# Kernel tuning notes

Measured on AMD Instinct MI355X. Metric: run time of the kernel, lower is better.

## Reference

```python
import jax, jax.numpy as jnp
import numpy as np

NUM_HEADS = 4
NUM_GROUPS = 32
EPS = 1e-5


def group_norm(x, gamma, beta):
    B, C, H, W = x.shape
    g = x.reshape(B, NUM_GROUPS, C // NUM_GROUPS, H, W)
    mean = g.mean(axis=(2, 3, 4), keepdims=True)
    var = g.var(axis=(2, 3, 4), keepdims=True)
    g = (g - mean) * jax.lax.rsqrt(var + EPS)
    x = g.reshape(B, C, H, W)
    return x * gamma[None, :, None, None] + beta[None, :, None, None]


def setup_inputs() -> dict:
    key = jax.random.key(0)
    ks = jax.random.split(key, 7)
    B, C, H, W = 16, 256, 32, 32
    x = jax.random.normal(ks[0], (B, C, H, W), dtype=jnp.float32)
    gn_gamma = jnp.ones((C,), dtype=jnp.float32)
    gn_beta = jnp.zeros((C,), dtype=jnp.float32)
    s = 1.0 / np.sqrt(C)
    qkv_w = jax.random.normal(ks[1], (3 * C, C), dtype=jnp.float32) * s
    qkv_b = jnp.zeros((3 * C,), dtype=jnp.float32)
    proj_w = jax.random.normal(ks[2], (C, C), dtype=jnp.float32) * s
    proj_b = jnp.zeros((C,), dtype=jnp.float32)
    return {"x": x, "gn_gamma": gn_gamma, "gn_beta": gn_beta,
            "qkv_w": qkv_w, "qkv_b": qkv_b, "proj_w": proj_w, "proj_b": proj_b}


def reference(x, gn_gamma, gn_beta, qkv_w, qkv_b, proj_w, proj_b):
    B, C, H, W = x.shape
    nh = NUM_HEADS
    d = C // nh
    N = H * W

    h = group_norm(x, gn_gamma, gn_beta)
    # 1x1 conv == channel matmul
    qkv = jnp.einsum('bchw,oc->bohw', h, qkv_w) + qkv_b[None, :, None, None]
    qkv = qkv.reshape(B, 3, nh, d, N)
    q, k, v = qkv[:, 0], qkv[:, 1], qkv[:, 2]  # each [B, nh, d, N]

    scale = 1.0 / jnp.sqrt(jnp.asarray(d, dtype=x.dtype))
    attn = jnp.einsum('bhdn,bhdm->bhnm', q, k) * scale  # [B, nh, N, N]
    attn = jax.nn.softmax(attn, axis=-1)
    out = jnp.einsum('bhnm,bhdm->bhdn', attn, v)  # [B, nh, d, N]
    out = out.reshape(B, C, H, W)

    out = jnp.einsum('bchw,oc->bohw', out, proj_w) + proj_b[None, :, None, None]
    return x + out
```

## Files before the change

kernel.cpp:

```cpp
#include <hip/hip_runtime.h>
#include <math.h>

typedef unsigned short u16;
typedef unsigned int u32;
typedef __attribute__((ext_vector_type(8))) short s16x8;
typedef __attribute__((ext_vector_type(4))) float f32x4;

#define NB 16
#define NN 1024
#define GN_EPS 1e-5f

static __device__ __forceinline__ u16 f2bf(float f) {
    union { float f; u32 u; } v; v.f = f;
    return (u16)((v.u + 0x8000u) >> 16);
}
static __device__ __forceinline__ u32 pk2(float a, float b) {
    union { float f; u32 u; } A, B; A.f = a; B.f = b;
    return __builtin_amdgcn_perm(A.u + 0x8000u, B.u + 0x8000u, 0x03020706u);
}

#define GLL16(gp, lp) __builtin_amdgcn_global_load_lds( \
    (const __attribute__((address_space(1))) void*)(const void*)(gp), \
    (__attribute__((address_space(3))) void*)(void*)(lp), 16, 0, 0)

__global__ __launch_bounds__(256) void gn_stats_kernel(
    const float* __restrict__ x, float2* __restrict__ stats)
{
    const int bg = blockIdx.x;
    const int t  = threadIdx.x;
    const float4* xb = (const float4*)(x + (size_t)bg * 8192);
    float s = 0.f, ss = 0.f;
#pragma unroll
    for (int i = 0; i < 8; ++i) {
        float4 f = xb[t + i * 256];
        s  += f.x + f.y + f.z + f.w;
        ss += f.x * f.x + f.y * f.y + f.z * f.z + f.w * f.w;
    }
#pragma unroll
    for (int off = 32; off > 0; off >>= 1) {
        s  += __shfl_down(s, off);
        ss += __shfl_down(ss, off);
    }
    __shared__ float red[8];
    const int wid = t >> 6;
    if ((t & 63) == 0) { red[wid] = s; red[4 + wid] = ss; }
    __syncthreads();
    if (t == 0) {
        float sa = red[0] + red[1] + red[2] + red[3];
        float sb = red[4] + red[5] + red[6] + red[7];
        float mean = sa * (1.0f / 8192.0f);
        float var  = sb * (1.0f / 8192.0f) - mean * mean;
        stats[bg] = make_float2(mean, 1.0f / sqrtf(var + GN_EPS));
    }
}

__global__ __launch_bounds__(256) void wcvt_kernel(
    const float* __restrict__ qkv_w, const float* __restrict__ proj_w,
    u16* __restrict__ wqb, u16* __restrict__ wpb)
{
    int i = blockIdx.x * 256 + threadIdx.x;
    if (i < 49152) {
        float4 f = ((const float4*)qkv_w)[i];
        *(uint2*)(wqb + (size_t)i * 4) = make_uint2(pk2(f.x, f.y), pk2(f.z, f.w));
    } else {
        int j = i - 49152;
        float4 f = ((const float4*)proj_w)[j];
        *(uint2*)(wpb + (size_t)j * 4) = make_uint2(pk2(f.x, f.y), pk2(f.z, f.w));
    }
}

__global__ __launch_bounds__(256) void gnorm_t_kernel(
    const float* __restrict__ x, const float2* __restrict__ stats,
    const float* __restrict__ gamma, const float* __restrict__ beta,
    u16* __restrict__ Xt)
{
    const int b = blockIdx.z, ct = blockIdx.y, nt = blockIdx.x;
    const int t = threadIdx.x;
    __shared__ float T[64][65];
    const float* xb = x + ((size_t)b * 256 + ct * 64) * NN + nt * 64;
#pragma unroll
    for (int i = 0; i < 4; ++i) {
        int row = i * 16 + (t >> 4), col = (t & 15) * 4;
        int ch = ct * 64 + row;
        float2 st = stats[b * 32 + (ch >> 3)];
        float gmv = st.y * gamma[ch];
        float btv = beta[ch] - st.x * gmv;
        float4 f = *(const float4*)&xb[(size_t)row * NN + col];
        T[row][col + 0] = f.x * gmv + btv;
        T[row][col + 1] = f.y * gmv + btv;
        T[row][col + 2] = f.z * gmv + btv;
        T[row][col + 3] = f.w * gmv + btv;
    }
    __syncthreads();
    u16* dst = Xt + ((size_t)b * NN + nt * 64) * 256 + ct * 64;
#pragma unroll
    for (int p = 0; p < 2; ++p) {
        int idx = t + p * 256;
        int nl = idx >> 3, c8 = idx & 7;
        s16x8 pv;
#pragma unroll
        for (int j = 0; j < 8; ++j) pv[j] = (short)f2bf(T[c8 * 8 + j][nl]);
        *(s16x8*)(dst + (size_t)nl * 256 + c8 * 8) = pv;
    }
}

__global__ __launch_bounds__(256) void qkv_mfma_kernel(
    const u16* __restrict__ Wb, const float* __restrict__ bias,
    const u16* __restrict__ Xt,
    u16* __restrict__ qh, u16* __restrict__ kh, u16* __restrict__ vh)
{
    const int b = blockIdx.z, ot = blockIdx.y, nt = blockIdx.x;
    const int t = threadIdx.x, w = t >> 6, l = t & 63;
    const int g = l >> 4, c = l & 15;
    __shared__ u16 Slds[32 * 512];
    const u16* Xb = Xt + ((size_t)b * NN + nt * 128) * 256;
    const u16* Wo = Wb + (size_t)ot * 64 * 256;
    const int part = ot >> 2, h = ot & 3;
    const size_t bhoff = (size_t)(b * 4 + h) << 16;

    if (part < 2) {
#pragma unroll
        for (int s = w; s < 32; s += 4) {
            int osub = s >> 3, ks = s & 7;
            GLL16(Wo + (size_t)(osub * 16 + c) * 256 + ks * 32 + g * 8, Slds + s * 512);
        }
        s16x8 a0[8], a1[8];
#pragma unroll
        for (int ks = 0; ks < 8; ++ks) {
            a0[ks] = *(const s16x8*)(Xb + (size_t)((2 * w) * 16 + c) * 256 + ks * 32 + g * 8);
            a1[ks] = *(const s16x8*)(Xb + (size_t)((2 * w + 1) * 16 + c) * 256 + ks * 32 + g * 8);
        }
        f32x4 acc[2][4];
#pragma unroll
        for (int i = 0; i < 2; ++i)
#pragma unroll
            for (int j = 0; j < 4; ++j) acc[i][j] = (f32x4){0.f, 0.f, 0.f, 0.f};
        __syncthreads();
#pragma unroll
        for (int ks = 0; ks < 8; ++ks)
#pragma unroll
            for (int j = 0; j < 4; ++j) {
                s16x8 bf = *(const s16x8*)(Slds + (j * 8 + ks) * 512 + l * 8);
                acc[0][j] = __builtin_amdgcn_mfma_f32_16x16x32_bf16(a0[ks], bf, acc[0][j], 0, 0, 0);
                acc[1][j] = __builtin_amdgcn_mfma_f32_16x16x32_bf16(a1[ks], bf, acc[1][j], 0, 0, 0);
            }
        const float sc = (part == 0) ? 0.125f * 1.44269504088896f : 1.0f;
        float bv[4];
#pragma unroll
        for (int j = 0; j < 4; ++j) bv[j] = bias[ot * 64 + j * 16 + c];
        u16* dst = (part == 0 ? qh : kh) + bhoff + (size_t)(nt * 128) * 64;
#pragma unroll
        for (int i = 0; i < 2; ++i)
#pragma unroll
            for (int j = 0; j < 4; ++j)
#pragma unroll
                for (int r = 0; r < 4; ++r) {
                    int n = (2 * w + i) * 16 + g * 4 + r;
                    dst[(size_t)n * 64 + j * 16 + c] = f2bf((acc[i][j][r] + bv[j]) * sc);
                }
    } else {
        f32x4 acc[8];
#pragma unroll
        for (int j = 0; j < 8; ++j) acc[j] = (f32x4){0.f, 0.f, 0.f, 0.f};
        for (int kk = 0; kk < 256; kk += 128) {
            if (kk) __syncthreads();
#pragma unroll
            for (int s = w; s < 32; s += 4) {
                int nsub = s >> 2, ks = s & 3;
                GLL16(Xb + (size_t)(nsub * 16 + c) * 256 + kk + ks * 32 + g * 8, Slds + s * 512);
            }
            __syncthreads();
#pragma unroll
            for (int ks = 0; ks < 4; ++ks) {
                s16x8 a = *(const s16x8*)(Wo + (size_t)(w * 16 + c) * 256 + kk + ks * 32 + g * 8);
#pragma unroll
                for (int j = 0; j < 8; ++j) {
                    s16x8 xf = *(const s16x8*)(Slds + (j * 4 + ks) * 512 + l * 8);
                    acc[j] = __builtin_amdgcn_mfma_f32_16x16x32_bf16(a, xf, acc[j], 0, 0, 0);
                }
            }
        }
        float bv[4];
#pragma unroll
        for (int r = 0; r < 4; ++r) bv[r] = bias[ot * 64 + w * 16 + g * 4 + r];
        u16* dst = vh + bhoff;
#pragma unroll
        for (int j = 0; j < 8; ++j)
#pragma unroll
            for (int r = 0; r < 4; ++r) {
                int d = w * 16 + g * 4 + r;
                int m = nt * 128 + j * 16 + c;
                dst[(size_t)d * NN + m] = f2bf(acc[j][r] + bv[r]);
            }
    }
}

__global__ __launch_bounds__(512) void attn_mfma_kernel(
    const u16* __restrict__ qh, const u16* __restrict__ kh,
    const u16* __restrict__ vh, u16* __restrict__ aoT)
{
    const int t = threadIdx.x;
    const int w = t >> 6, l = t & 63;
    const int g = l >> 4, c = l & 15;
    const int bid = blockIdx.x;
    const int xcd = bid & 7;
    const int idx = bid >> 3;
    const int qt  = idx & 7;
    const int grp = (idx >> 3) * 8 + xcd;
    const int b = grp >> 2, h = grp & 3;
    const size_t bhoff = (size_t)grp << 16;
    const int n_base = qt * 128 + w * 16;

    __shared__ u16 Klds[2][8 * 512];
    __shared__ u16 Vlds[2][8 * 512];
    __shared__ u16 Plds[8][2 * 512];

    const u16* qb = qh + bhoff;
    const u16* kb = kh + bhoff;
    const u16* vb = vh + bhoff;

    const int msub = w >> 1, uu = w & 1;

    s16x8 qf[2];
#pragma unroll
    for (int u = 0; u < 2; ++u)
        qf[u] = *(const s16x8*)(qb + (size_t)(n_base + c) * 64 + u * 32 + g * 8);

    s16x8 onef;
#pragma unroll
    for (int j = 0; j < 8; ++j) onef[j] = (short)0x3F80;

    f32x4 Oacc[4];
    f32x4 Lacc = (f32x4){0.f, 0.f, 0.f, 0.f};
#pragma unroll
    for (int ds = 0; ds < 4; ++ds) Oacc[ds] = (f32x4){0.f, 0.f, 0.f, 0.f};

    u16* pw = &Plds[w][0];

    GLL16(kb + (size_t)(msub * 16 + c) * 64 + uu * 32 + g * 8, &Klds[0][w * 512]);
    GLL16(vb + (size_t)(msub * 16 + c) * NN + uu * 32 + g * 8, &Vlds[0][w * 512]);

    for (int mt = 0; mt < 16; ++mt) {
        const int cur = mt & 1;
        if (mt < 15) {
            const int m1 = (mt + 1) * 64;
            GLL16(kb + (size_t)(m1 + msub * 16 + c) * 64 + uu * 32 + g * 8, &Klds[cur ^ 1][w * 512]);
            GLL16(vb + (size_t)(msub * 16 + c) * NN + m1 + uu * 32 + g * 8, &Vlds[cur ^ 1][w * 512]);
            asm volatile("s_waitcnt vmcnt(2)" ::: "memory");
        } else {
            asm volatile("s_waitcnt vmcnt(0)" ::: "memory");
        }
        __builtin_amdgcn_s_barrier();
        asm volatile("" ::: "memory");

        const u16* Kc = &Klds[cur][0];
        const u16* Vc = &Vlds[cur][0];

        f32x4 S[4];
#pragma unroll
        for (int ms = 0; ms < 4; ++ms) S[ms] = (f32x4){0.f, 0.f, 0.f, 0.f};
#pragma unroll
        for (int ms = 0; ms < 4; ++ms)
#pragma unroll
            for (int u = 0; u < 2; ++u) {
                s16x8 af = *(const s16x8*)(Kc + (ms * 2 + u) * 512 + l * 8);
                S[ms] = __builtin_amdgcn_mfma_f32_16x16x32_bf16(af, qf[u], S[ms], 0, 0, 0);
            }

        s16x8 vf[4][2];
#pragma unroll
        for (int ds = 0; ds < 4; ++ds)
#pragma unroll
            for (int u = 0; u < 2; ++u)
                vf[ds][u] = *(const s16x8*)(Vc + (ds * 2 + u) * 512 + l * 8);

#pragma unroll
        for (int ms = 0; ms < 4; ++ms)
#pragma unroll
            for (int r = 0; r < 4; ++r) S[ms][r] = __builtin_amdgcn_exp2f(S[ms][r]);

#pragma unroll
        for (int ms = 0; ms < 4; ++ms) {
            u32 d0 = pk2(S[ms][0], S[ms][1]);
            u32 d1 = pk2(S[ms][2], S[ms][3]);
            int off = (ms >> 1) * 512 + ((ms & 1) * 2 + (g >> 1)) * 128 + c * 8 + (g & 1) * 4;
            *(uint2*)(pw + off) = make_uint2(d0, d1);
        }
        asm volatile("s_waitcnt lgkmcnt(0)" ::: "memory");
#pragma unroll
        for (int u = 0; u < 2; ++u) {
            s16x8 pf = *(const s16x8*)(pw + u * 512 + l * 8);
#pragma unroll
            for (int ds = 0; ds < 4; ++ds)
                Oacc[ds] = __builtin_amdgcn_mfma_f32_16x16x32_bf16(vf[ds][u], pf, Oacc[ds], 0, 0, 0);
            Lacc = __builtin_amdgcn_mfma_f32_16x16x32_bf16(onef, pf, Lacc, 0, 0, 0);
        }
        asm volatile("" ::: "memory");
        __builtin_amdgcn_s_barrier();
    }

    u16* aob = aoT + (size_t)b * NN * 256 + h * 64;
    float inv = 1.0f / Lacc[0];
    const size_t nrow = (size_t)(n_base + c) * 256;
#pragma unroll
    for (int ds = 0; ds < 4; ++ds) {
        u32 lo = pk2(Oacc[ds][0] * inv, Oacc[ds][1] * inv);
        u32 hi = pk2(Oacc[ds][2] * inv, Oacc[ds][3] * inv);
        *(uint2*)(aob + nrow + ds * 16 + g * 4) = make_uint2(lo, hi);
    }
}

__global__ __launch_bounds__(256) void proj_mfma_kernel(
    const u16* __restrict__ Wb, const float* __restrict__ bias,
    const u16* __restrict__ aoT, const float* __restrict__ x,
    float* __restrict__ out)
{
    const int b = blockIdx.z, ot = blockIdx.y, nt = blockIdx.x;
    const int t = threadIdx.x, w = t >> 6, l = t & 63;
    const int g = l >> 4, c = l & 15;
    __shared__ u16 Slds[32 * 512];
    const u16* Xb = aoT + ((size_t)b * NN + nt * 128) * 256;
    const u16* Wo = Wb + (size_t)ot * 64 * 256;

    f32x4 acc[8];
#pragma unroll
    for (int j = 0; j < 8; ++j) acc[j] = (f32x4){0.f, 0.f, 0.f, 0.f};
    for (int kk = 0; kk < 256; kk += 128) {
        if (kk) __syncthreads();
#pragma unroll
        for (int s = w; s < 32; s += 4) {
            int nsub = s >> 2, ks = s & 3;
            GLL16(Xb + (size_t)(nsub * 16 + c) * 256 + kk + ks * 32 + g * 8, Slds + s * 512);
        }
        __syncthreads();
#pragma unroll
        for (int ks = 0; ks < 4; ++ks) {
            s16x8 a = *(const s16x8*)(Wo + (size_t)(w * 16 + c) * 256 + kk + ks * 32 + g * 8);
#pragma unroll
            for (int j = 0; j < 8; ++j) {
                s16x8 xf = *(const s16x8*)(Slds + (j * 4 + ks) * 512 + l * 8);
                acc[j] = __builtin_amdgcn_mfma_f32_16x16x32_bf16(a, xf, acc[j], 0, 0, 0);
            }
        }
    }
    float bv[4];
#pragma unroll
    for (int r = 0; r < 4; ++r) bv[r] = bias[ot * 64 + w * 16 + g * 4 + r];
#pragma unroll
    for (int j = 0; j < 8; ++j)
#pragma unroll
        for (int r = 0; r < 4; ++r) {
            int o = ot * 64 + w * 16 + g * 4 + r;
            int n = nt * 128 + j * 16 + c;
            size_t addr = ((size_t)b * 256 + o) * NN + n;
            out[addr] = acc[j][r] + bv[r] + x[addr];
        }
}

extern "C" void kernel_launch(void* const* d_in, const int* in_sizes, int n_in,
                              void* d_out, int out_size, void* d_ws, size_t ws_size,
                              hipStream_t stream)
{
    const float* x      = (const float*)d_in[0];
    const float* gamma  = (const float*)d_in[1];
    const float* beta   = (const float*)d_in[2];
    const float* qkv_w  = (const float*)d_in[3];
    const float* qkv_b  = (const float*)d_in[4];
    const float* proj_w = (const float*)d_in[5];
    const float* proj_b = (const float*)d_in[6];
    float* out = (float*)d_out;

    float* ws = (float*)d_ws;
    float2* stats = (float2*)ws;
    u16* Xt  = (u16*)(ws + 1024);
    u16* wqb = Xt + (size_t)4194304;
    u16* wpb = wqb + (size_t)196608;
    u16* qh  = wpb + (size_t)65536;
    u16* kh  = qh + (size_t)4194304;
    u16* vh  = kh + (size_t)4194304;
    u16* aoT = vh + (size_t)4194304;

    gn_stats_kernel<<<dim3(NB * 32), 256, 0, stream>>>(x, stats);
    wcvt_kernel<<<dim3(256), 256, 0, stream>>>(qkv_w, proj_w, wqb, wpb);
    gnorm_t_kernel<<<dim3(16, 4, NB), 256, 0, stream>>>(x, stats, gamma, beta, Xt);

    qkv_mfma_kernel<<<dim3(8, 12, NB), 256, 0, stream>>>(
        wqb, qkv_b, Xt, qh, kh, vh);

    attn_mfma_kernel<<<dim3(512), 512, 0, stream>>>(qh, kh, vh, aoT);

    proj_mfma_kernel<<<dim3(8, 4, NB), 256, 0, stream>>>(
        wpb, proj_b, aoT, x, out);
}
```

Measured before the change: 84.42 us.

## Deepen attention K/V pipeline to four buffers and use hardware bf16 pack

The attention kernel moves from a double-buffered K/V LDS pipeline to four buffers. It prefetches two 64-key tiles at a time and processes two tiles per barrier pair, so there are half as many barriers and more loads in flight. The manual rounding-and-permute bf16 packing is replaced by the v_cvt_pk_bf16_f32 instruction, and the explicit lgkmcnt wait before reading P back is dropped. It also adds a launch-bounds occupancy hint. The trade-offs are that LDS use rises to about 80KB per block, and the occupancy hint may squeeze registers and cause spills.

```diff
diff --git a/kernel.cpp b/kernel.cpp
--- a/kernel.cpp
+++ b/kernel.cpp
@@ -17,6 +17,11 @@
 static __device__ __forceinline__ u32 pk2(float a, float b) {
     union { float f; u32 u; } A, B; A.f = a; B.f = b;
     return __builtin_amdgcn_perm(A.u + 0x8000u, B.u + 0x8000u, 0x03020706u);
+}
+static __device__ __forceinline__ u32 cvtpk2(float a, float b) {
+    u32 r;
+    asm("v_cvt_pk_bf16_f32 %0, %1, %2" : "=v"(r) : "v"(a), "v"(b));
+    return r;
 }
 
 #define GLL16(gp, lp) __builtin_amdgcn_global_load_lds( \
@@ -195,7 +200,7 @@
     }
 }
 
-__global__ __launch_bounds__(512) void attn_mfma_kernel(
+__global__ __launch_bounds__(512, 4) void attn_mfma_kernel(
     const u16* __restrict__ qh, const u16* __restrict__ kh,
     const u16* __restrict__ vh, u16* __restrict__ aoT)
 {
@@ -211,8 +216,8 @@
     const size_t bhoff = (size_t)grp << 16;
     const int n_base = qt * 128 + w * 16;
 
-    __shared__ u16 Klds[2][8 * 512];
-    __shared__ u16 Vlds[2][8 * 512];
+    __shared__ u16 Klds[4][8 * 512];
+    __shared__ u16 Vlds[4][8 * 512];
     __shared__ u16 Plds[8][2 * 512];
 
     const u16* qb = qh + bhoff;
@@ -237,25 +242,12 @@
 
     u16* pw = &Plds[w][0];
 
-    GLL16(kb + (size_t)(msub * 16 + c) * 64 + uu * 32 + g * 8, &Klds[0][w * 512]);
-    GLL16(vb + (size_t)(msub * 16 + c) * NN + uu * 32 + g * 8, &Vlds[0][w * 512]);
-
-    for (int mt = 0; mt < 16; ++mt) {
-        const int cur = mt & 1;
-        if (mt < 15) {
-            const int m1 = (mt + 1) * 64;
-            GLL16(kb + (size_t)(m1 + msub * 16 + c) * 64 + uu * 32 + g * 8, &Klds[cur ^ 1][w * 512]);
-            GLL16(vb + (size_t)(msub * 16 + c) * NN + m1 + uu * 32 + g * 8, &Vlds[cur ^ 1][w * 512]);
-            asm volatile("s_waitcnt vmcnt(2)" ::: "memory");
-        } else {
-            asm volatile("s_waitcnt vmcnt(0)" ::: "memory");
-        }
-        __builtin_amdgcn_s_barrier();
-        asm volatile("" ::: "memory");
-
-        const u16* Kc = &Klds[cur][0];
-        const u16* Vc = &Vlds[cur][0];
-
+#define STK(tt) GLL16(kb + (size_t)((tt) * 64 + msub * 16 + c) * 64 + uu * 32 + g * 8, &Klds[(tt) & 3][w * 512])
+#define STV(tt) GLL16(vb + (size_t)(msub * 16 + c) * NN + (tt) * 64 + uu * 32 + g * 8, &Vlds[(tt) & 3][w * 512])
+
+    auto tile = [&](int buf) {
+        const u16* Kc = &Klds[buf][0];
+        const u16* Vc = &Vlds[buf][0];
         f32x4 S[4];
 #pragma unroll
         for (int ms = 0; ms < 4; ++ms) S[ms] = (f32x4){0.f, 0.f, 0.f, 0.f};
@@ -266,27 +258,23 @@
                 s16x8 af = *(const s16x8*)(Kc + (ms * 2 + u) * 512 + l * 8);
                 S[ms] = __builtin_amdgcn_mfma_f32_16x16x32_bf16(af, qf[u], S[ms], 0, 0, 0);
             }
-
         s16x8 vf[4][2];
 #pragma unroll
         for (int ds = 0; ds < 4; ++ds)
 #pragma unroll
             for (int u = 0; u < 2; ++u)
                 vf[ds][u] = *(const s16x8*)(Vc + (ds * 2 + u) * 512 + l * 8);
-
 #pragma unroll
         for (int ms = 0; ms < 4; ++ms)
 #pragma unroll
             for (int r = 0; r < 4; ++r) S[ms][r] = __builtin_amdgcn_exp2f(S[ms][r]);
-
 #pragma unroll
         for (int ms = 0; ms < 4; ++ms) {
-            u32 d0 = pk2(S[ms][0], S[ms][1]);
-            u32 d1 = pk2(S[ms][2], S[ms][3]);
+            u32 d0 = cvtpk2(S[ms][0], S[ms][1]);
+            u32 d1 = cvtpk2(S[ms][2], S[ms][3]);
             int off = (ms >> 1) * 512 + ((ms & 1) * 2 + (g >> 1)) * 128 + c * 8 + (g & 1) * 4;
             *(uint2*)(pw + off) = make_uint2(d0, d1);
         }
-        asm volatile("s_waitcnt lgkmcnt(0)" ::: "memory");
 #pragma unroll
         for (int u = 0; u < 2; ++u) {
             s16x8 pf = *(const s16x8*)(pw + u * 512 + l * 8);
@@ -295,6 +283,24 @@
                 Oacc[ds] = __builtin_amdgcn_mfma_f32_16x16x32_bf16(vf[ds][u], pf, Oacc[ds], 0, 0, 0);
             Lacc = __builtin_amdgcn_mfma_f32_16x16x32_bf16(onef, pf, Lacc, 0, 0, 0);
         }
+    };
+
+    STK(0); STV(0); STK(1); STV(1);
+
+    for (int it = 0; it < 8; ++it) {
+        if (it < 7) {
+            STK(2 * it + 2); STV(2 * it + 2);
+            STK(2 * it + 3); STV(2 * it + 3);
+            asm volatile("s_waitcnt vmcnt(4)" ::: "memory");
+        } else {
+            asm volatile("s_waitcnt vmcnt(0)" ::: "memory");
+        }
+        __builtin_amdgcn_s_barrier();
+        asm volatile("" ::: "memory");
+
+        tile((2 * it) & 3);
+        tile((2 * it + 1) & 3);
+
         asm volatile("" ::: "memory");
         __builtin_amdgcn_s_barrier();
     }
@@ -304,10 +310,12 @@
     const size_t nrow = (size_t)(n_base + c) * 256;
 #pragma unroll
     for (int ds = 0; ds < 4; ++ds) {
-        u32 lo = pk2(Oacc[ds][0] * inv, Oacc[ds][1] * inv);
-        u32 hi = pk2(Oacc[ds][2] * inv, Oacc[ds][3] * inv);
+        u32 lo = cvtpk2(Oacc[ds][0] * inv, Oacc[ds][1] * inv);
+        u32 hi = cvtpk2(Oacc[ds][2] * inv, Oacc[ds][3] * inv);
         *(uint2*)(aob + nrow + ds * 16 + g * 4) = make_uint2(lo, hi);
     }
+#undef STK
+#undef STV
 }
 
 __global__ __launch_bounds__(256) void proj_mfma_kernel(
```

Result: no change. 83.33 us (-1.3%).
